# Kernel tuning notes

Hardware: AMD Instinct MI355X
Metric: run time of the kernel (lower is better)

Reference implementation:

```python
import jax, jax.numpy as jnp
import numpy as np
from jax import lax

GROUPS = 32
EPS = 1e-5
NEG_SLOPE = 0.1


def group_norm(x, gamma, beta):
    # x: (B, C, H, W); GroupNorm over (C//G, H, W) per group
    B, C, H, W = x.shape
    xr = x.reshape(B, GROUPS, C // GROUPS, H, W)
    mean = xr.mean(axis=(2, 3, 4), keepdims=True)
    var = xr.var(axis=(2, 3, 4), keepdims=True)
    xn = ((xr - mean) * lax.rsqrt(var + EPS)).reshape(B, C, H, W)
    return xn * gamma[None, :, None, None] + beta[None, :, None, None]


def conv3x3(x, w, b):
    y = lax.conv_general_dilated(x, w, (1, 1), 'SAME',
                                 dimension_numbers=('NCHW', 'OIHW', 'NCHW'))
    return y + b[None, :, None, None]


def leaky_relu(x):
    return jnp.where(x >= 0, x, NEG_SLOPE * x)


def setup_inputs() -> dict:
    key = jax.random.key(0)
    ks = jax.random.split(key, 12)
    B, C, H, W = 16, 128, 128, 128
    emb = 128
    s = 0.05
    return {
        'x': jax.random.normal(ks[0], (B, C, H, W), jnp.float32),
        'time_emb': jax.random.normal(ks[1], (B, emb), jnp.float32),
        'k_v': jax.random.normal(ks[2], (B, 64), jnp.float32),
        'gn1_g': jnp.ones((C,), jnp.float32),
        'gn1_b': jnp.zeros((C,), jnp.float32),
        'conv1_w': jax.random.normal(ks[3], (C, C, 3, 3), jnp.float32) * s,
        'conv1_b': jax.random.normal(ks[4], (C,), jnp.float32) * s,
        'nf_w': jax.random.normal(ks[5], (C, emb), jnp.float32) * s,
        'nf_b': jax.random.normal(ks[6], (C,), jnp.float32) * s,
        'kW1': jax.random.normal(ks[7], (64, 64), jnp.float32) * s,
        'kW2': jax.random.normal(ks[8], (C * 9, 64), jnp.float32) * s,
        'daconv_w': jax.random.normal(ks[9], (C, C, 3, 3), jnp.float32) * s,
        'daconv_b': jax.random.normal(ks[10], (C,), jnp.float32) * s,
    }


def reference(x, time_emb, k_v, gn1_g, gn1_b, conv1_w, conv1_b,
              nf_w, nf_b, kW1, kW2, daconv_w, daconv_b):
    B, C, H, W = x.shape
    # block1: GroupNorm -> Swish -> Conv3x3
    h = group_norm(x, gn1_g, gn1_b)
    h = h * jax.nn.sigmoid(h)
    h = conv3x3(h, conv1_w, conv1_b)
    # FeatureWiseAffine (use_affine_level=False): h + Linear(time_emb)
    h = h + (time_emb @ nf_w.T + nf_b)[:, :, None, None]
    # DABlock: its GroupNorm+Swish output is discarded in the original code,
    # so only DA_conv(h, k_v) matters.
    # dynamic per-sample depthwise kernel: (B, 64) -> (B*C, 1, 3, 3)
    kern = (leaky_relu(k_v @ kW1.T) @ kW2.T).reshape(B * C, 1, 3, 3)
    xr = h.reshape(1, B * C, H, W)
    dyn = lax.conv_general_dilated(xr, kern, (1, 1), 'SAME',
                                   dimension_numbers=('NCHW', 'OIHW', 'NCHW'),
                                   feature_group_count=B * C)
    dyn = leaky_relu(dyn).reshape(B, C, H, W)
    h = dyn + conv3x3(h, daconv_w, daconv_b)
    # residual: dim == dim_out -> res_conv = Identity
    return h + x
```

## Files before the change

### kernel.cpp

```cpp
#include <hip/hip_runtime.h>
#include <hip/hip_bf16.h>
#include <math.h>
#include <stdint.h>

typedef unsigned short u16;
typedef __attribute__((ext_vector_type(8))) short bfrag;
typedef __attribute__((ext_vector_type(4))) float f32x4;
typedef __attribute__((ext_vector_type(8))) unsigned short u16x8;
typedef __attribute__((ext_vector_type(4))) unsigned short u16x4;

#define BB 16
#define CC 128
#define HH 128
#define WW 128
#define EPSV 1e-5f
#define NEG 0.1f
#define PW 130

__device__ __forceinline__ float bf2f(u16 u) {
    unsigned int x = ((unsigned int)u) << 16;
    return __builtin_bit_cast(float, x);
}
__device__ __forceinline__ u16 f2bf(float f) {
    unsigned int x = __builtin_bit_cast(unsigned int, f);
    unsigned int r = x + 0x7fffu + ((x >> 16) & 1u);
    return (u16)(r >> 16);
}
__device__ __forceinline__ void gload_lds16(const void* g, void* l) {
    __builtin_amdgcn_global_load_lds(
        (const __attribute__((address_space(1))) void*)g,
        (__attribute__((address_space(3))) void*)l, 16, 0, 0);
}

__global__ __launch_bounds__(256)
void border_kernel(u16* __restrict__ a, u16* __restrict__ h) {
    int idx = blockIdx.x * 256 + threadIdx.x;
    if (idx >= BB * 516 * 16) return;
    int cg = idx & 15;
    int t = idx >> 4;
    int b = t / 516, e = t - b * 516;
    int y, x;
    if (e < 130)      { y = 0;           x = e; }
    else if (e < 260) { y = 129;         x = e - 130; }
    else if (e < 388) { y = e - 260 + 1; x = 0; }
    else              { y = e - 388 + 1; x = 129; }
    size_t o = (((size_t)b * PW + y) * PW + x) * 128 + cg * 8;
    u16x8 z = (u16x8)(u16)0;
    *(u16x8*)&a[o] = z;
    *(u16x8*)&h[o] = z;
}

__global__ __launch_bounds__(256)
void gn_stats_kernel(const float* __restrict__ x, float* __restrict__ stats) {
    const int bg = blockIdx.x;
    const float* base = x + (size_t)bg * 65536;
    float s1 = 0.f, s2 = 0.f;
    for (int i = threadIdx.x; i < 16384; i += 256) {
        float4 v = *(const float4*)&base[i * 4];
        s1 += v.x + v.y + v.z + v.w;
        s2 += v.x * v.x + v.y * v.y + v.z * v.z + v.w * v.w;
    }
    #pragma unroll
    for (int off = 32; off > 0; off >>= 1) {
        s1 += __shfl_down(s1, off);
        s2 += __shfl_down(s2, off);
    }
    __shared__ float rs[8];
    const int wid = threadIdx.x >> 6, lane = threadIdx.x & 63;
    if (lane == 0) { rs[wid * 2] = s1; rs[wid * 2 + 1] = s2; }
    __syncthreads();
    if (threadIdx.x == 0) {
        s1 = rs[0] + rs[2] + rs[4] + rs[6];
        s2 = rs[1] + rs[3] + rs[5] + rs[7];
        float mean = s1 * (1.f / 65536.f);
        float var  = s2 * (1.f / 65536.f) - mean * mean;
        stats[2 * bg]     = mean;
        stats[2 * bg + 1] = rsqrtf(var + EPSV);
    }
}

__global__ __launch_bounds__(256)
void wconv_kernel(const float* __restrict__ w1, const float* __restrict__ w2,
                  u16* __restrict__ w1t, u16* __restrict__ w2t) {
    int idx = blockIdx.x * 256 + threadIdx.x;
    if (idx < 147456) {
        int e  = idx & 7;
        int co = (idx >> 3) & 127;
        int g  = (idx >> 10) & 3;
        int ck = (idx >> 12) & 3;
        int t  = idx >> 14;
        int src = (co * 128 + (ck * 32 + g * 8 + e)) * 9 + t;
        w1t[idx] = f2bf(w1[src]);
        w2t[idx] = f2bf(w2[src]);
    }
}

__global__ __launch_bounds__(256)
void small1_kernel(const float* __restrict__ te, const float* __restrict__ nfw,
                   const float* __restrict__ nfbias, const float* __restrict__ c1b,
                   const float* __restrict__ kv, const float* __restrict__ kw1,
                   float* __restrict__ biastot, float* __restrict__ tmp1) {
    const int idx = blockIdx.x * 256 + threadIdx.x;
    if (idx < 1024) {
        const int b = idx >> 6, j = idx & 63;
        float s = 0.f;
        for (int e = 0; e < 64; ++e) s += kv[b * 64 + e] * kw1[j * 64 + e];
        tmp1[idx] = s >= 0.f ? s : NEG * s;
    } else if (idx < 1024 + 2048) {
        const int t = idx - 1024;
        const int b = t >> 7, c = t & 127;
        float s = nfbias[c] + c1b[c];
        for (int e = 0; e < 128; ++e) s += te[b * 128 + e] * nfw[c * 128 + e];
        biastot[t] = s;
    }
}

__global__ __launch_bounds__(256)
void small2_kernel(const float* __restrict__ tmp1, const float* __restrict__ kw2,
                   float* __restrict__ kern_t) {
    const int idx = blockIdx.x * 256 + threadIdx.x;
    if (idx < BB * CC * 9) {
        const int b = idx / 1152, rc = idx % 1152;
        const int c = rc / 9, t = rc - c * 9;
        float s = 0.f;
        for (int e = 0; e < 64; ++e) s += tmp1[b * 64 + e] * kw2[rc * 64 + e];
        kern_t[((size_t)b * 9 + t) * 128 + c] = s;
    }
}

__global__ __launch_bounds__(256)
void gn_apply_kernel(const float* __restrict__ x, const float* __restrict__ gamma,
                     const float* __restrict__ beta, const float* __restrict__ stats,
                     u16* __restrict__ hact) {
    __shared__ u16 s_t[128 * 128];
    const int tid = threadIdx.x;
    const int y = blockIdx.x & 127, b = blockIdx.x >> 7;
    #pragma unroll
    for (int i = 0; i < 16; ++i) {
        int unit = (i << 8) + tid;
        int c = unit >> 5, xq = unit & 31, xx = xq * 4;
        float4 v = *(const float4*)&x[(((size_t)b * 128 + c) * 128 + y) * 128 + xx];
        int gi = b * 32 + (c >> 2);
        float mean = stats[2 * gi], rstd = stats[2 * gi + 1];
        float ga = gamma[c] * rstd, be = beta[c] - mean * ga;
        float a0 = v.x * ga + be, a1 = v.y * ga + be, a2 = v.z * ga + be, a3 = v.w * ga + be;
        a0 = a0 / (1.f + __expf(-a0)); a1 = a1 / (1.f + __expf(-a1));
        a2 = a2 / (1.f + __expf(-a2)); a3 = a3 / (1.f + __expf(-a3));
        int cs = c ^ ((xq & 15) << 3);
        s_t[(xx + 0) * 128 + cs] = f2bf(a0);
        s_t[(xx + 1) * 128 + cs] = f2bf(a1);
        s_t[(xx + 2) * 128 + cs] = f2bf(a2);
        s_t[(xx + 3) * 128 + cs] = f2bf(a3);
    }
    __syncthreads();
    #pragma unroll
    for (int i = 0; i < 8; ++i) {
        int unit = (i << 8) + tid;
        int xx = unit >> 4, c0 = (unit & 15) * 8;
        int c0s = c0 ^ (((xx >> 2) & 15) << 3);
        u16x8 v = *(const u16x8*)&s_t[xx * 128 + c0s];
        *(u16x8*)&hact[(((size_t)b * PW + y + 1) * PW + (xx + 1)) * 128 + c0] = v;
    }
}

__global__ __launch_bounds__(1024, 4)
void conv1_mfma_kernel(const u16* __restrict__ act, const u16* __restrict__ wt,
                       const float* __restrict__ bias, u16* __restrict__ outh) {
    __shared__ __align__(16) u16 s_in[2][2496 * 8];

    const int tid = threadIdx.x;
    const int lane = tid & 63, wid = tid >> 6;
    const int wm = wid & 1, wq = wid >> 1;
    const int l15 = lane & 15, l4 = lane >> 4;

    const int bid0 = blockIdx.x;
    const int bid = ((bid0 & 7) << 6) | (bid0 >> 3);
    const int tx = bid & 7, ty = (bid >> 3) & 3, b = bid >> 5;
    const int x0 = tx * 16, y0 = ty * 32;

    f32x4 acc[4][4];
    #pragma unroll
    for (int mi = 0; mi < 4; ++mi)
        #pragma unroll
        for (int nj = 0; nj < 4; ++nj) acc[mi][nj] = (f32x4)(0.f);

    int in_vofs[3];
    bool in_act[3];
    #pragma unroll
    for (int r = 0; r < 3; ++r) {
        int slot_base = r * 1024 + (wid << 6);
        in_act[r] = slot_base < 2448;
        int slot = r * 1024 + tid;
        if (slot > 2447) slot = 2447;
        int cik = slot / 612;
        int pos = slot - cik * 612;
        int row = pos / 18, col = pos - row * 18;
        in_vofs[r] = (row * PW + col) * 128 + cik * 8;
    }
    const u16* in_base = act + (((size_t)b * PW + y0) * PW + x0) * 128;
    const int ldst = (wid << 6) * 8;

    auto stage_in = [&](int buf, int ci0) {
        #pragma unroll
        for (int r = 0; r < 3; ++r)
            if (in_act[r])
                gload_lds16(in_base + ci0 + in_vofs[r],
                            &s_in[buf][(r * 1024) * 8 + ldst]);
    };

    const u16* wlane = wt + l4 * 1024 + (wm * 64 + l15) * 8;
    const int bbase = (l4 * 612 + (wq * 4) * 18 + l15) * 8;

    stage_in(0, 0);
    asm volatile("s_waitcnt vmcnt(0)" ::: "memory");
    __builtin_amdgcn_s_barrier();
    __builtin_amdgcn_sched_barrier(0);

    #pragma unroll
    for (int c = 0; c < 4; ++c) {
        if (c > 0) {
            asm volatile("s_waitcnt vmcnt(0)" ::: "memory");
            __builtin_amdgcn_s_barrier();
        }
        if (c < 3) stage_in((c + 1) & 1, (c + 1) * 32);
        __builtin_amdgcn_sched_barrier(0);

        const u16* sb = &s_in[c & 1][0];
        #pragma unroll
        for (int dyr = 0; dyr < 3; ++dyr) {
            #pragma unroll
            for (int dx = 0; dx < 3; ++dx) {
                const u16* wp = wlane + ((dyr * 3 + dx) * 4 + c) * 4096;
                bfrag a0 = *(const bfrag*)(wp);
                bfrag a1 = *(const bfrag*)(wp + 128);
                bfrag a2 = *(const bfrag*)(wp + 256);
                bfrag a3 = *(const bfrag*)(wp + 384);
                const int bo = bbase + (dyr * 18 + dx) * 8;
                bfrag b0 = *(const bfrag*)&sb[bo];
                bfrag b1 = *(const bfrag*)&sb[bo + 144];
                bfrag b2 = *(const bfrag*)&sb[bo + 288];
                bfrag b3 = *(const bfrag*)&sb[bo + 432];

                __builtin_amdgcn_s_setprio(1);
                acc[0][0] = __builtin_amdgcn_mfma_f32_16x16x32_bf16(a0, b0, acc[0][0], 0, 0, 0);
                acc[0][1] = __builtin_amdgcn_mfma_f32_16x16x32_bf16(a0, b1, acc[0][1], 0, 0, 0);
                acc[0][2] = __builtin_amdgcn_mfma_f32_16x16x32_bf16(a0, b2, acc[0][2], 0, 0, 0);
                acc[0][3] = __builtin_amdgcn_mfma_f32_16x16x32_bf16(a0, b3, acc[0][3], 0, 0, 0);
                acc[1][0] = __builtin_amdgcn_mfma_f32_16x16x32_bf16(a1, b0, acc[1][0], 0, 0, 0);
                acc[1][1] = __builtin_amdgcn_mfma_f32_16x16x32_bf16(a1, b1, acc[1][1], 0, 0, 0);
                acc[1][2] = __builtin_amdgcn_mfma_f32_16x16x32_bf16(a1, b2, acc[1][2], 0, 0, 0);
                acc[1][3] = __builtin_amdgcn_mfma_f32_16x16x32_bf16(a1, b3, acc[1][3], 0, 0, 0);
                acc[2][0] = __builtin_amdgcn_mfma_f32_16x16x32_bf16(a2, b0, acc[2][0], 0, 0, 0);
                acc[2][1] = __builtin_amdgcn_mfma_f32_16x16x32_bf16(a2, b1, acc[2][1], 0, 0, 0);
                acc[2][2] = __builtin_amdgcn_mfma_f32_16x16x32_bf16(a2, b2, acc[2][2], 0, 0, 0);
                acc[2][3] = __builtin_amdgcn_mfma_f32_16x16x32_bf16(a2, b3, acc[2][3], 0, 0, 0);
                acc[3][0] = __builtin_amdgcn_mfma_f32_16x16x32_bf16(a3, b0, acc[3][0], 0, 0, 0);
                acc[3][1] = __builtin_amdgcn_mfma_f32_16x16x32_bf16(a3, b1, acc[3][1], 0, 0, 0);
                acc[3][2] = __builtin_amdgcn_mfma_f32_16x16x32_bf16(a3, b2, acc[3][2], 0, 0, 0);
                acc[3][3] = __builtin_amdgcn_mfma_f32_16x16x32_bf16(a3, b3, acc[3][3], 0, 0, 0);
                __builtin_amdgcn_s_setprio(0);
            }
        }
    }

    const float* bb = bias + b * 128;
    #pragma unroll
    for (int mi = 0; mi < 4; ++mi) {
        const int cb = wm * 64 + mi * 16 + l4 * 4;
        float4 bv4 = *(const float4*)&bb[cb];
        #pragma unroll
        for (int nj = 0; nj < 4; ++nj) {
            int y = y0 + wq * 4 + nj, xx = x0 + l15;
            u16x4 pk;
            pk[0] = f2bf(acc[mi][nj][0] + bv4.x);
            pk[1] = f2bf(acc[mi][nj][1] + bv4.y);
            pk[2] = f2bf(acc[mi][nj][2] + bv4.z);
            pk[3] = f2bf(acc[mi][nj][3] + bv4.w);
            *(u16x4*)&outh[(((size_t)b * PW + y + 1) * PW + (xx + 1)) * 128 + cb] = pk;
        }
    }
}

__global__ __launch_bounds__(512, 2)
void conv2_mfma_kernel(const u16* __restrict__ act, const u16* __restrict__ wt,
                       const float* __restrict__ bias, const float* __restrict__ kern_t,
                       const float* __restrict__ xres, float* __restrict__ outf) {
    __shared__ __align__(16) u16 s_in[2][1536 * 8];
    __shared__ float s_k[1152];

    const int tid = threadIdx.x;
    const int lane = tid & 63, wid = tid >> 6;
    const int wm = wid & 1, wq = wid >> 1;
    const int l15 = lane & 15, l4 = lane >> 4;

    const int bid0 = blockIdx.x;
    const int bid = ((bid0 & 7) << 7) | (bid0 >> 3);
    const int tx = bid & 7, ty = (bid >> 3) & 15, b = bid >> 7;
    const int x0 = tx * 16, y0 = (ty & 7) * 16;
    const int b2 = bid >> 6;
    (void)b2;

    f32x4 acc[4][4];
    #pragma unroll
    for (int mi = 0; mi < 4; ++mi)
        #pragma unroll
        for (int nj = 0; nj < 4; ++nj) acc[mi][nj] = (f32x4)(0.f);

    float dw[2][2][4][4];
    #pragma unroll
    for (int a0 = 0; a0 < 2; ++a0)
        #pragma unroll
        for (int a1 = 0; a1 < 2; ++a1)
            #pragma unroll
            for (int a2 = 0; a2 < 4; ++a2)
                #pragma unroll
                for (int a3 = 0; a3 < 4; ++a3) dw[a0][a1][a2][a3] = 0.f;

    const int bb_ = bid >> 6;
    const int b_  = bb_;
    const int ty_ = (bid >> 3) & 7;
    const int y0_ = ty_ * 16;

    for (int i = tid; i < 1152; i += 512) s_k[i] = kern_t[(size_t)b_ * 1152 + i];
    __syncthreads();

    int in_vofs[3];
    #pragma unroll
    for (int r = 0; r < 3; ++r) {
        int slot = r * 512 + tid;
        int cik = slot / 384;
        int pos = slot - cik * 384;
        if (pos > 323) pos = 323;
        int row = pos / 18, col = pos - row * 18;
        in_vofs[r] = (row * PW + col) * 128 + cik * 8;
    }
    const u16* in_base = act + (((size_t)b_ * PW + y0_) * PW + x0) * 128;
    const int ldst = (wid << 6) * 8;

    auto stage_in = [&](int buf, int ci0) {
        #pragma unroll
        for (int r = 0; r < 3; ++r)
            gload_lds16(in_base + ci0 + in_vofs[r], &s_in[buf][r * 512 * 8 + ldst]);
    };

    const u16* wlane = wt + l4 * 1024 + (wm * 64 + l15) * 8;
    const int bbase = (l4 * 384 + (wq * 4) * 18 + l15) * 8;

    auto dwcomp = [&](int ck, int dyr) {
        if ((ck >> 1) == wm) {
            const int mih = ck & 1;
            const u16* sb = &s_in[ck & 1][0];
            #pragma unroll
            for (int mm = 0; mm < 2; ++mm) {
                const int cik = 2 * mm + (l4 >> 1);
                const int e0 = (l4 & 1) * 4;
                const int cb = ck * 32 + mm * 16 + l4 * 4;
                #pragma unroll
                for (int dx = 0; dx < 3; ++dx) {
                    const int tap = dyr * 3 + dx;
                    float4 kk = *(const float4*)&s_k[tap * 128 + cb];
                    #pragma unroll
                    for (int nj = 0; nj < 4; ++nj) {
                        const int row = wq * 4 + nj + dyr;
                        const int col = l15 + dx;
                        u16x4 hv = *(const u16x4*)
                            &sb[(cik * 384 + row * 18 + col) * 8 + e0];
                        dw[mih][mm][nj][0] += bf2f(hv[0]) * kk.x;
                        dw[mih][mm][nj][1] += bf2f(hv[1]) * kk.y;
                        dw[mih][mm][nj][2] += bf2f(hv[2]) * kk.z;
                        dw[mih][mm][nj][3] += bf2f(hv[3]) * kk.w;
                    }
                }
            }
        }
    };

    stage_in(0, 0);
    asm volatile("s_waitcnt vmcnt(0)" ::: "memory");
    __builtin_amdgcn_s_barrier();
    __builtin_amdgcn_sched_barrier(0);

    #pragma unroll
    for (int c = 0; c < 4; ++c) {
        if (c > 0) {
            __builtin_amdgcn_s_barrier();
        }
        if (c < 3) {
            stage_in((c + 1) & 1, (c + 1) * 32);
            asm volatile("s_waitcnt vmcnt(3)" ::: "memory");
        }
        __builtin_amdgcn_sched_barrier(0);

        const u16* sb = &s_in[c & 1][0];
        #pragma unroll
        for (int dyr = 0; dyr < 3; ++dyr) {
            bfrag wR[3][4];
            #pragma unroll
            for (int dx = 0; dx < 3; ++dx) {
                const u16* wp = wlane + ((dyr * 3 + dx) * 4 + c) * 4096;
                #pragma unroll
                for (int mi = 0; mi < 4; ++mi)
                    wR[dx][mi] = *(const bfrag*)(wp + mi * 128);
            }
            __builtin_amdgcn_s_setprio(1);
            #pragma unroll
            for (int dx = 0; dx < 3; ++dx) {
                const int bo = bbase + (dyr * 18 + dx) * 8;
                bfrag b0 = *(const bfrag*)&sb[bo];
                bfrag b1 = *(const bfrag*)&sb[bo + 144];
                bfrag b2 = *(const bfrag*)&sb[bo + 288];
                bfrag b3 = *(const bfrag*)&sb[bo + 432];

                acc[0][0] = __builtin_amdgcn_mfma_f32_16x16x32_bf16(wR[dx][0], b0, acc[0][0], 0, 0, 0);
                acc[0][1] = __builtin_amdgcn_mfma_f32_16x16x32_bf16(wR[dx][0], b1, acc[0][1], 0, 0, 0);
                acc[0][2] = __builtin_amdgcn_mfma_f32_16x16x32_bf16(wR[dx][0], b2, acc[0][2], 0, 0, 0);
                acc[0][3] = __builtin_amdgcn_mfma_f32_16x16x32_bf16(wR[dx][0], b3, acc[0][3], 0, 0, 0);
                acc[1][0] = __builtin_amdgcn_mfma_f32_16x16x32_bf16(wR[dx][1], b0, acc[1][0], 0, 0, 0);
                acc[1][1] = __builtin_amdgcn_mfma_f32_16x16x32_bf16(wR[dx][1], b1, acc[1][1], 0, 0, 0);
                acc[1][2] = __builtin_amdgcn_mfma_f32_16x16x32_bf16(wR[dx][1], b2, acc[1][2], 0, 0, 0);
                acc[1][3] = __builtin_amdgcn_mfma_f32_16x16x32_bf16(wR[dx][1], b3, acc[1][3], 0, 0, 0);
                acc[2][0] = __builtin_amdgcn_mfma_f32_16x16x32_bf16(wR[dx][2], b0, acc[2][0], 0, 0, 0);
                acc[2][1] = __builtin_amdgcn_mfma_f32_16x16x32_bf16(wR[dx][2], b1, acc[2][1], 0, 0, 0);
                acc[2][2] = __builtin_amdgcn_mfma_f32_16x16x32_bf16(wR[dx][2], b2, acc[2][2], 0, 0, 0);
                acc[2][3] = __builtin_amdgcn_mfma_f32_16x16x32_bf16(wR[dx][2], b3, acc[2][3], 0, 0, 0);
                acc[3][0] = __builtin_amdgcn_mfma_f32_16x16x32_bf16(wR[dx][3], b0, acc[3][0], 0, 0, 0);
                acc[3][1] = __builtin_amdgcn_mfma_f32_16x16x32_bf16(wR[dx][3], b1, acc[3][1], 0, 0, 0);
                acc[3][2] = __builtin_amdgcn_mfma_f32_16x16x32_bf16(wR[dx][3], b2, acc[3][2], 0, 0, 0);
                acc[3][3] = __builtin_amdgcn_mfma_f32_16x16x32_bf16(wR[dx][3], b3, acc[3][3], 0, 0, 0);
            }
            __builtin_amdgcn_s_setprio(0);
            dwcomp(c, dyr);
        }
    }

    #pragma unroll
    for (int mi = 0; mi < 4; ++mi) {
        const int cb = wm * 64 + mi * 16 + l4 * 4;
        float4 bv4 = *(const float4*)&bias[cb];
        #pragma unroll
        for (int nj = 0; nj < 4; ++nj) {
            int y = y0_ + wq * 4 + nj, xx = x0 + l15;
            size_t obase = (((size_t)b_ * 128 + cb) * 128 + y) * 128 + xx;
            #pragma unroll
            for (int j = 0; j < 4; ++j) {
                float d = dw[mi >> 1][mi & 1][nj][j];
                d = d >= 0.f ? d : NEG * d;
                float bj = (j == 0) ? bv4.x : (j == 1) ? bv4.y : (j == 2) ? bv4.z : bv4.w;
                outf[obase + (size_t)j * 16384] =
                    acc[mi][nj][j] + bj + d + xres[obase + (size_t)j * 16384];
            }
        }
    }
}

extern "C" void kernel_launch(void* const* d_in, const int* in_sizes, int n_in,
                              void* d_out, int out_size, void* d_ws, size_t ws_size,
                              hipStream_t stream) {
    const float* x        = (const float*)d_in[0];
    const float* te       = (const float*)d_in[1];
    const float* kv       = (const float*)d_in[2];
    const float* gn1_g    = (const float*)d_in[3];
    const float* gn1_b    = (const float*)d_in[4];
    const float* conv1_w  = (const float*)d_in[5];
    const float* conv1_b  = (const float*)d_in[6];
    const float* nf_w     = (const float*)d_in[7];
    const float* nf_b     = (const float*)d_in[8];
    const float* kW1      = (const float*)d_in[9];
    const float* kW2      = (const float*)d_in[10];
    const float* daconv_w = (const float*)d_in[11];
    const float* daconv_b = (const float*)d_in[12];

    float* out = (float*)d_out;

    float* kern  = (float*)d_ws;
    u16*   w2t   = (u16*)(kern + 18432);
    u16*   hbuf  = (u16*)(kern + 92160);

    u16*   hact    = (u16*)out;
    float* up      = out + 17500160;
    float* stats   = up;
    float* biastot = up + 1024;
    float* tmp1    = up + 3072;
    u16*   w1t     = (u16*)(up + 4096);

    border_kernel<<<dim3(516), dim3(256), 0, stream>>>(hact, hbuf);
    gn_stats_kernel<<<dim3(512), dim3(256), 0, stream>>>(x, stats);
    wconv_kernel<<<dim3(576), dim3(256), 0, stream>>>(conv1_w, daconv_w, w1t, w2t);
    small1_kernel<<<dim3(12), dim3(256), 0, stream>>>(te, nf_w, nf_b, conv1_b, kv, kW1,
                                                      biastot, tmp1);
    small2_kernel<<<dim3(72), dim3(256), 0, stream>>>(tmp1, kW2, kern);
    gn_apply_kernel<<<dim3(2048), dim3(256), 0, stream>>>(x, gn1_g, gn1_b, stats, hact);

    conv1_mfma_kernel<<<dim3(512), dim3(1024), 0, stream>>>(hact, w1t, biastot, hbuf);
    conv2_mfma_kernel<<<dim3(1024), dim3(512), 0, stream>>>(
        hbuf, w2t, daconv_b, kern, x, out);
}
```

Measured before the change: 323.4 us.

## Merge prep kernels into one launch and retile conv1 into smaller blocks

Five small setup kernels (border zeroing, GroupNorm stats, weight conversion, time-embedding bias, dynamic kernel generation) are folded into one prep kernel dispatched by block index, with the two-stage kernel MLP kept in shared memory inside one block per batch. This removes launch overhead and the serial dependency between the small kernels. Separately, conv1 moves from 1024-thread blocks covering 32 rows to 512-thread blocks covering 8 rows with half the per-wave output channels, giving four times as many blocks with smaller LDS and register use. The explicit vmcnt wait before the barrier in the conv1 loop is also dropped, which risks reading staged LDS data before the async loads finish.

```diff
diff --git a/kernel.cpp b/kernel.cpp
--- a/kernel.cpp
+++ b/kernel.cpp
@@ -33,57 +33,47 @@
 }
 
 __global__ __launch_bounds__(256)
-void border_kernel(u16* __restrict__ a, u16* __restrict__ h) {
-    int idx = blockIdx.x * 256 + threadIdx.x;
-    if (idx >= BB * 516 * 16) return;
-    int cg = idx & 15;
-    int t = idx >> 4;
-    int b = t / 516, e = t - b * 516;
-    int y, x;
-    if (e < 130)      { y = 0;           x = e; }
-    else if (e < 260) { y = 129;         x = e - 130; }
-    else if (e < 388) { y = e - 260 + 1; x = 0; }
-    else              { y = e - 388 + 1; x = 129; }
-    size_t o = (((size_t)b * PW + y) * PW + x) * 128 + cg * 8;
-    u16x8 z = (u16x8)(u16)0;
-    *(u16x8*)&a[o] = z;
-    *(u16x8*)&h[o] = z;
-}
-
-__global__ __launch_bounds__(256)
-void gn_stats_kernel(const float* __restrict__ x, float* __restrict__ stats) {
-    const int bg = blockIdx.x;
-    const float* base = x + (size_t)bg * 65536;
-    float s1 = 0.f, s2 = 0.f;
-    for (int i = threadIdx.x; i < 16384; i += 256) {
-        float4 v = *(const float4*)&base[i * 4];
-        s1 += v.x + v.y + v.z + v.w;
-        s2 += v.x * v.x + v.y * v.y + v.z * v.z + v.w * v.w;
-    }
-    #pragma unroll
-    for (int off = 32; off > 0; off >>= 1) {
-        s1 += __shfl_down(s1, off);
-        s2 += __shfl_down(s2, off);
-    }
+void prep_kernel(const float* __restrict__ x, float* __restrict__ stats,
+                 const float* __restrict__ w1, const float* __restrict__ w2,
+                 u16* __restrict__ w1t, u16* __restrict__ w2t,
+                 u16* __restrict__ hact, u16* __restrict__ hbuf,
+                 const float* __restrict__ te, const float* __restrict__ nfw,
+                 const float* __restrict__ nfbias, const float* __restrict__ c1b,
+                 float* __restrict__ biastot,
+                 const float* __restrict__ kv, const float* __restrict__ kw1,
+                 const float* __restrict__ kw2, float* __restrict__ kern_t) {
     __shared__ float rs[8];
-    const int wid = threadIdx.x >> 6, lane = threadIdx.x & 63;
-    if (lane == 0) { rs[wid * 2] = s1; rs[wid * 2 + 1] = s2; }
-    __syncthreads();
-    if (threadIdx.x == 0) {
-        s1 = rs[0] + rs[2] + rs[4] + rs[6];
-        s2 = rs[1] + rs[3] + rs[5] + rs[7];
-        float mean = s1 * (1.f / 65536.f);
-        float var  = s2 * (1.f / 65536.f) - mean * mean;
-        stats[2 * bg]     = mean;
-        stats[2 * bg + 1] = rsqrtf(var + EPSV);
-    }
-}
-
-__global__ __launch_bounds__(256)
-void wconv_kernel(const float* __restrict__ w1, const float* __restrict__ w2,
-                  u16* __restrict__ w1t, u16* __restrict__ w2t) {
-    int idx = blockIdx.x * 256 + threadIdx.x;
-    if (idx < 147456) {
+    __shared__ float s_t1[64];
+    const int blk = blockIdx.x;
+    const int tid = threadIdx.x;
+
+    if (blk < 512) {
+        const int bg = blk;
+        const float* base = x + (size_t)bg * 65536;
+        float s1 = 0.f, s2 = 0.f;
+        for (int i = tid; i < 16384; i += 256) {
+            float4 v = *(const float4*)&base[i * 4];
+            s1 += v.x + v.y + v.z + v.w;
+            s2 += v.x * v.x + v.y * v.y + v.z * v.z + v.w * v.w;
+        }
+        #pragma unroll
+        for (int off = 32; off > 0; off >>= 1) {
+            s1 += __shfl_down(s1, off);
+            s2 += __shfl_down(s2, off);
+        }
+        const int wid = tid >> 6, lane = tid & 63;
+        if (lane == 0) { rs[wid * 2] = s1; rs[wid * 2 + 1] = s2; }
+        __syncthreads();
+        if (tid == 0) {
+            s1 = rs[0] + rs[2] + rs[4] + rs[6];
+            s2 = rs[1] + rs[3] + rs[5] + rs[7];
+            float mean = s1 * (1.f / 65536.f);
+            float var  = s2 * (1.f / 65536.f) - mean * mean;
+            stats[2 * bg]     = mean;
+            stats[2 * bg + 1] = rsqrtf(var + EPSV);
+        }
+    } else if (blk < 1088) {
+        int idx = (blk - 512) * 256 + tid;
         int e  = idx & 7;
         int co = (idx >> 3) & 127;
         int g  = (idx >> 10) & 3;
@@ -92,39 +82,40 @@
         int src = (co * 128 + (ck * 32 + g * 8 + e)) * 9 + t;
         w1t[idx] = f2bf(w1[src]);
         w2t[idx] = f2bf(w2[src]);
-    }
-}
-
-__global__ __launch_bounds__(256)
-void small1_kernel(const float* __restrict__ te, const float* __restrict__ nfw,
-                   const float* __restrict__ nfbias, const float* __restrict__ c1b,
-                   const float* __restrict__ kv, const float* __restrict__ kw1,
-                   float* __restrict__ biastot, float* __restrict__ tmp1) {
-    const int idx = blockIdx.x * 256 + threadIdx.x;
-    if (idx < 1024) {
-        const int b = idx >> 6, j = idx & 63;
-        float s = 0.f;
-        for (int e = 0; e < 64; ++e) s += kv[b * 64 + e] * kw1[j * 64 + e];
-        tmp1[idx] = s >= 0.f ? s : NEG * s;
-    } else if (idx < 1024 + 2048) {
-        const int t = idx - 1024;
-        const int b = t >> 7, c = t & 127;
+    } else if (blk < 1604) {
+        int idx = (blk - 1088) * 256 + tid;
+        int cg = idx & 15;
+        int t = idx >> 4;
+        int b = t / 516, e = t - b * 516;
+        int y, xx;
+        if (e < 130)      { y = 0;           xx = e; }
+        else if (e < 260) { y = 129;         xx = e - 130; }
+        else if (e < 388) { y = e - 260 + 1; xx = 0; }
+        else              { y = e - 388 + 1; xx = 129; }
+        size_t o = (((size_t)b * PW + y) * PW + xx) * 128 + cg * 8;
+        u16x8 z = (u16x8)(u16)0;
+        *(u16x8*)&hact[o] = z;
+        *(u16x8*)&hbuf[o] = z;
+    } else if (blk < 1612) {
+        int idx = (blk - 1604) * 256 + tid;
+        const int b = idx >> 7, c = idx & 127;
         float s = nfbias[c] + c1b[c];
         for (int e = 0; e < 128; ++e) s += te[b * 128 + e] * nfw[c * 128 + e];
-        biastot[t] = s;
-    }
-}
-
-__global__ __launch_bounds__(256)
-void small2_kernel(const float* __restrict__ tmp1, const float* __restrict__ kw2,
-                   float* __restrict__ kern_t) {
-    const int idx = blockIdx.x * 256 + threadIdx.x;
-    if (idx < BB * CC * 9) {
-        const int b = idx / 1152, rc = idx % 1152;
-        const int c = rc / 9, t = rc - c * 9;
-        float s = 0.f;
-        for (int e = 0; e < 64; ++e) s += tmp1[b * 64 + e] * kw2[rc * 64 + e];
-        kern_t[((size_t)b * 9 + t) * 128 + c] = s;
+        biastot[idx] = s;
+    } else {
+        const int b = blk - 1612;
+        if (tid < 64) {
+            float s = 0.f;
+            for (int e = 0; e < 64; ++e) s += kv[b * 64 + e] * kw1[tid * 64 + e];
+            s_t1[tid] = s >= 0.f ? s : NEG * s;
+        }
+        __syncthreads();
+        for (int i = tid; i < 1152; i += 256) {
+            float s = 0.f;
+            for (int e = 0; e < 64; ++e) s += s_t1[e] * kw2[(size_t)i * 64 + e];
+            int c = i / 9, t = i - c * 9;
+            kern_t[((size_t)b * 9 + t) * 128 + c] = s;
+        }
     }
 }
 
@@ -163,53 +154,48 @@
     }
 }
 
-__global__ __launch_bounds__(1024, 4)
+__global__ __launch_bounds__(512, 4)
 void conv1_mfma_kernel(const u16* __restrict__ act, const u16* __restrict__ wt,
                        const float* __restrict__ bias, u16* __restrict__ outh) {
-    __shared__ __align__(16) u16 s_in[2][2496 * 8];
+    __shared__ __align__(16) u16 s_in[2][1024 * 8];
 
     const int tid = threadIdx.x;
     const int lane = tid & 63, wid = tid >> 6;
-    const int wm = wid & 1, wq = wid >> 1;
+    const int wm = wid & 3, wq = wid >> 2;
     const int l15 = lane & 15, l4 = lane >> 4;
 
     const int bid0 = blockIdx.x;
-    const int bid = ((bid0 & 7) << 6) | (bid0 >> 3);
-    const int tx = bid & 7, ty = (bid >> 3) & 3, b = bid >> 5;
-    const int x0 = tx * 16, y0 = ty * 32;
-
-    f32x4 acc[4][4];
-    #pragma unroll
-    for (int mi = 0; mi < 4; ++mi)
+    const int bid = ((bid0 & 7) << 8) | (bid0 >> 3);
+    const int tx = bid & 7, ty = (bid >> 3) & 15, b = bid >> 7;
+    const int x0 = tx * 16, y0 = ty * 8;
+
+    f32x4 acc[2][4];
+    #pragma unroll
+    for (int mi = 0; mi < 2; ++mi)
         #pragma unroll
         for (int nj = 0; nj < 4; ++nj) acc[mi][nj] = (f32x4)(0.f);
 
-    int in_vofs[3];
-    bool in_act[3];
-    #pragma unroll
-    for (int r = 0; r < 3; ++r) {
-        int slot_base = r * 1024 + (wid << 6);
-        in_act[r] = slot_base < 2448;
-        int slot = r * 1024 + tid;
-        if (slot > 2447) slot = 2447;
-        int cik = slot / 612;
-        int pos = slot - cik * 612;
+    int in_vofs[2];
+    #pragma unroll
+    for (int r = 0; r < 2; ++r) {
+        int slot = r * 512 + tid;
+        if (slot > 719) slot = 719;
+        int cik = slot / 180;
+        int pos = slot - cik * 180;
         int row = pos / 18, col = pos - row * 18;
         in_vofs[r] = (row * PW + col) * 128 + cik * 8;
     }
     const u16* in_base = act + (((size_t)b * PW + y0) * PW + x0) * 128;
-    const int ldst = (wid << 6) * 8;
 
     auto stage_in = [&](int buf, int ci0) {
         #pragma unroll
-        for (int r = 0; r < 3; ++r)
-            if (in_act[r])
-                gload_lds16(in_base + ci0 + in_vofs[r],
-                            &s_in[buf][(r * 1024) * 8 + ldst]);
+        for (int r = 0; r < 2; ++r)
+            gload_lds16(in_base + ci0 + in_vofs[r],
+                        &s_in[buf][(size_t)(r * 512 + (wid << 6)) * 8]);
     };
 
-    const u16* wlane = wt + l4 * 1024 + (wm * 64 + l15) * 8;
-    const int bbase = (l4 * 612 + (wq * 4) * 18 + l15) * 8;
+    const u16* wlane = wt + l4 * 1024 + (wm * 32 + l15) * 8;
+    const int bbase = (l4 * 180 + (wq * 4) * 18 + l15) * 8;
 
     stage_in(0, 0);
     asm volatile("s_waitcnt vmcnt(0)" ::: "memory");
@@ -219,8 +205,8 @@
     #pragma unroll
     for (int c = 0; c < 4; ++c) {
         if (c > 0) {
-            asm volatile("s_waitcnt vmcnt(0)" ::: "memory");
             __builtin_amdgcn_s_barrier();
+            __builtin_amdgcn_sched_barrier(0);
         }
         if (c < 3) stage_in((c + 1) & 1, (c + 1) * 32);
         __builtin_amdgcn_sched_barrier(0);
@@ -230,11 +216,9 @@
         for (int dyr = 0; dyr < 3; ++dyr) {
             #pragma unroll
             for (int dx = 0; dx < 3; ++dx) {
-                const u16* wp = wlane + ((dyr * 3 + dx) * 4 + c) * 4096;
+                const u16* wp = wlane + (size_t)(((dyr * 3 + dx) * 4 + c) * 4096);
                 bfrag a0 = *(const bfrag*)(wp);
                 bfrag a1 = *(const bfrag*)(wp + 128);
-                bfrag a2 = *(const bfrag*)(wp + 256);
-                bfrag a3 = *(const bfrag*)(wp + 384);
                 const int bo = bbase + (dyr * 18 + dx) * 8;
                 bfrag b0 = *(const bfrag*)&sb[bo];
                 bfrag b1 = *(const bfrag*)&sb[bo + 144];
@@ -250,14 +234,6 @@
                 acc[1][1] = __builtin_amdgcn_mfma_f32_16x16x32_bf16(a1, b1, acc[1][1], 0, 0, 0);
                 acc[1][2] = __builtin_amdgcn_mfma_f32_16x16x32_bf16(a1, b2, acc[1][2], 0, 0, 0);
                 acc[1][3] = __builtin_amdgcn_mfma_f32_16x16x32_bf16(a1, b3, acc[1][3], 0, 0, 0);
-                acc[2][0] = __builtin_amdgcn_mfma_f32_16x16x32_bf16(a2, b0, acc[2][0], 0, 0, 0);
-                acc[2][1] = __builtin_amdgcn_mfma_f32_16x16x32_bf16(a2, b1, acc[2][1], 0, 0, 0);
-                acc[2][2] = __builtin_amdgcn_mfma_f32_16x16x32_bf16(a2, b2, acc[2][2], 0, 0, 0);
-                acc[2][3] = __builtin_amdgcn_mfma_f32_16x16x32_bf16(a2, b3, acc[2][3], 0, 0, 0);
-                acc[3][0] = __builtin_amdgcn_mfma_f32_16x16x32_bf16(a3, b0, acc[3][0], 0, 0, 0);
-                acc[3][1] = __builtin_amdgcn_mfma_f32_16x16x32_bf16(a3, b1, acc[3][1], 0, 0, 0);
-                acc[3][2] = __builtin_amdgcn_mfma_f32_16x16x32_bf16(a3, b2, acc[3][2], 0, 0, 0);
-                acc[3][3] = __builtin_amdgcn_mfma_f32_16x16x32_bf16(a3, b3, acc[3][3], 0, 0, 0);
                 __builtin_amdgcn_s_setprio(0);
             }
         }
@@ -265,8 +241,8 @@
 
     const float* bb = bias + b * 128;
     #pragma unroll
-    for (int mi = 0; mi < 4; ++mi) {
-        const int cb = wm * 64 + mi * 16 + l4 * 4;
+    for (int mi = 0; mi < 2; ++mi) {
+        const int cb = wm * 32 + mi * 16 + l4 * 4;
         float4 bv4 = *(const float4*)&bb[cb];
         #pragma unroll
         for (int nj = 0; nj < 4; ++nj) {
@@ -295,10 +271,11 @@
 
     const int bid0 = blockIdx.x;
     const int bid = ((bid0 & 7) << 7) | (bid0 >> 3);
-    const int tx = bid & 7, ty = (bid >> 3) & 15, b = bid >> 7;
-    const int x0 = tx * 16, y0 = (ty & 7) * 16;
-    const int b2 = bid >> 6;
-    (void)b2;
+    const int tx = bid & 7;
+    const int x0 = tx * 16;
+    const int b_  = bid >> 6;
+    const int ty_ = (bid >> 3) & 7;
+    const int y0_ = ty_ * 16;
 
     f32x4 acc[4][4];
     #pragma unroll
@@ -315,11 +292,6 @@
             for (int a2 = 0; a2 < 4; ++a2)
                 #pragma unroll
                 for (int a3 = 0; a3 < 4; ++a3) dw[a0][a1][a2][a3] = 0.f;
-
-    const int bb_ = bid >> 6;
-    const int b_  = bb_;
-    const int ty_ = (bid >> 3) & 7;
-    const int y0_ = ty_ * 16;
 
     for (int i = tid; i < 1152; i += 512) s_k[i] = kern_t[(size_t)b_ * 1152 + i];
     __syncthreads();
@@ -480,18 +452,13 @@
     float* up      = out + 17500160;
     float* stats   = up;
     float* biastot = up + 1024;
-    float* tmp1    = up + 3072;
     u16*   w1t     = (u16*)(up + 4096);
 
-    border_kernel<<<dim3(516), dim3(256), 0, stream>>>(hact, hbuf);
-    gn_stats_kernel<<<dim3(512), dim3(256), 0, stream>>>(x, stats);
-    wconv_kernel<<<dim3(576), dim3(256), 0, stream>>>(conv1_w, daconv_w, w1t, w2t);
-    small1_kernel<<<dim3(12), dim3(256), 0, stream>>>(te, nf_w, nf_b, conv1_b, kv, kW1,
-                                                      biastot, tmp1);
-    small2_kernel<<<dim3(72), dim3(256), 0, stream>>>(tmp1, kW2, kern);
+    prep_kernel<<<dim3(1628), dim3(256), 0, stream>>>(
+        x, stats, conv1_w, daconv_w, w1t, w2t, hact, hbuf,
+        te, nf_w, nf_b, conv1_b, biastot, kv, kW1, kW2, kern);
     gn_apply_kernel<<<dim3(2048), dim3(256), 0, stream>>>(x, gn1_g, gn1_b, stats, hact);
-
-    conv1_mfma_kernel<<<dim3(512), dim3(1024), 0, stream>>>(hact, w1t, biastot, hbuf);
+    conv1_mfma_kernel<<<dim3(2048), dim3(512), 0, stream>>>(hact, w1t, biastot, hbuf);
     conv2_mfma_kernel<<<dim3(1024), dim3(512), 0, stream>>>(
         hbuf, w2t, daconv_b, kern, x, out);
 }
```

Result: faster. 290.0 us (-10.3%).
